# Kernel optimization log

Hardware: AMD Instinct MI355X
Metric: run time of the kernel (lower is better)

The kernel has to match this reference:

```python
import jax, jax.numpy as jnp
import numpy as np

RADIUS = 0.2
MAX_SAMPLES = 32  # max_samples_per_query


def ball_query(coords, queries, radius, k):
    """coords: [B,Np,3], queries: [B,Nq,3] -> idxs: [B,Nq,k] (first-k in index order,
    empty slots filled with the first valid index, or 0 if no neighbor -- matches
    the standard PointNet++ CUDA ball_query semantics)."""
    Np = coords.shape[1]
    # squared distances [B, Nq, Np]
    diff = queries[:, :, None, :] - coords[:, None, :, :]
    d2 = jnp.sum(diff * diff, axis=-1)
    mask = d2 < radius * radius
    # keys: point index if in-ball else sentinel Np; smallest k keys = first k valid indices
    keys = jnp.where(mask, jnp.arange(Np, dtype=jnp.int32), Np)
    neg_top, _ = jax.lax.top_k(-keys, k)           # largest of -keys == smallest keys
    sorted_keys = -neg_top                          # [B, Nq, k], ascending
    valid = sorted_keys < Np
    first = jnp.where(valid[..., 0:1], sorted_keys[..., 0:1], 0)
    return jnp.where(valid, sorted_keys, first)


def setup_inputs() -> dict:
    key = jax.random.key(0)
    k1, k2, k3, k4 = jax.random.split(key, 4)
    B, Np, Nq, C, Ct = 4, 8192, 2048, 64, 64
    return {
        "points_coords": jax.random.uniform(k1, (B, Np, 3), dtype=jnp.float32),
        "points_features": jax.random.normal(k2, (B, C, Np), dtype=jnp.float32),
        "points_t_embed": jax.random.normal(k3, (B, Ct, Np), dtype=jnp.float32),
        "queries": jax.random.uniform(k4, (B, Nq, 3), dtype=jnp.float32),
    }


def reference(points_coords, points_features, points_t_embed, queries):
    B, Np, _ = points_coords.shape
    Nq = queries.shape[1]
    K = MAX_SAMPLES
    idxs = ball_query(points_coords, queries, RADIUS, K)          # [B,Nq,K] int32
    flat = idxs.reshape(B, Nq * K)
    # grouped coords: gather along point dim then center on queries -> [B,Nq,K,3]
    grouped_coords = jnp.take_along_axis(points_coords, flat[:, :, None], axis=1)
    grouped_coords = grouped_coords.reshape(B, Nq, K, 3) - queries[:, :, None, :]
    # grouped features: gather channel-first along point dim -> [B,C,Nq,K]
    C = points_features.shape[1]
    grouped_features = jnp.take_along_axis(points_features, flat[:, None, :], axis=2)
    grouped_features = grouped_features.reshape(B, C, Nq, K)
    # use_coords=True: prepend centered coords as channels
    grouped_features = jnp.concatenate(
        [grouped_coords.transpose(0, 3, 1, 2), grouped_features], axis=1)  # [B,3+C,Nq,K]
    # t_embed gather -> [B,Ct,Nq,K]
    Ct = points_t_embed.shape[1]
    t_embed = jnp.take_along_axis(points_t_embed, flat[:, None, :], axis=2)
    t_embed = t_embed.reshape(B, Ct, Nq, K)
    return grouped_features, t_embed
```

## Files before the change

### kernel.cpp

```cpp
#include <hip/hip_runtime.h>

constexpr int kB  = 4;
constexpr int kNp = 8192;
constexpr int kNq = 2048;
constexpr int kK  = 32;
constexpr float kR2 = (float)(0.2 * 0.2);

__global__ __launch_bounds__(256) void coords_soa_kernel(
    const float* __restrict__ coords, float* __restrict__ cb3)
{
    const int t = blockIdx.x * 256 + threadIdx.x;
    const int b = t >> 13;
    const int p = t & (kNp - 1);
    const float x = coords[(size_t)t * 3 + 0];
    const float y = coords[(size_t)t * 3 + 1];
    const float z = coords[(size_t)t * 3 + 2];
    float* o = cb3 + (size_t)b * 3 * kNp;
    o[0 * kNp + p] = x;
    o[1 * kNp + p] = y;
    o[2 * kNp + p] = z;
}

__global__ __launch_bounds__(256) void ball_query_kernel(
    const float* __restrict__ cb3,
    const float* __restrict__ queries,
    int* __restrict__ idxs,
    float* __restrict__ out)
{
    const int wave = (int)((blockIdx.x * blockDim.x + threadIdx.x) >> 6);
    const int lane = threadIdx.x & 63;
    const int w    = threadIdx.x >> 6;
    const int b    = wave >> 11;
    const int q    = wave & (kNq - 1);

    const float qx = queries[(b * kNq + q) * 3 + 0];
    const float qy = queries[(b * kNq + q) * 3 + 1];
    const float qz = queries[(b * kNq + q) * 3 + 2];

    const float* __restrict__ cbx = cb3 + (size_t)b * 3 * kNp;
    const float* __restrict__ cby = cbx + kNp;
    const float* __restrict__ cbz = cby + kNp;

    __shared__ int s_idx[4][kK];

    const unsigned long long lt = (1ull << lane) - 1ull;
    int cnt = 0;
    for (int base = 0; base < kNp; base += 256) {
#pragma unroll
        for (int j = 0; j < 4; ++j) {
            const int p = base + j * 64 + lane;
            const float cx = cbx[p];
            const float cy = cby[p];
            const float cz = cbz[p];
            const float dx = __fsub_rn(qx, cx);
            const float dy = __fsub_rn(qy, cy);
            const float dz = __fsub_rn(qz, cz);
            const float d2 = __fadd_rn(
                __fadd_rn(__fmul_rn(dx, dx), __fmul_rn(dy, dy)),
                __fmul_rn(dz, dz));
            const bool in_ball = d2 < kR2;
            const unsigned long long m = __ballot(in_ball);
            if (in_ball) {
                const int slot = cnt + __popcll(m & lt);
                if (slot < kK) s_idx[w][slot] = p;
            }
            cnt += __popcll(m);
        }
        if (cnt >= kK) break;
    }

    if (lane < kK) {
        int v;
        if (cnt == 0)        v = 0;
        else if (lane < cnt) v = s_idx[w][lane];
        else                 v = s_idx[w][0];
        idxs[(size_t)wave * kK + lane] = v;

        const int k = lane;
        float* gf = out + ((size_t)(b * 67) * kNq + q) * kK + k;
        gf[(size_t)0 * kNq * kK] = __fsub_rn(cbx[v], qx);
        gf[(size_t)1 * kNq * kK] = __fsub_rn(cby[v], qy);
        gf[(size_t)2 * kNq * kK] = __fsub_rn(cbz[v], qz);
    }
}

__global__ __launch_bounds__(256) void gather_kernel(
    const float* __restrict__ feat,
    const float* __restrict__ temb,
    const int*   __restrict__ idxs,
    float* __restrict__ out)
{
    const int blk = blockIdx.x;
    const int b   = blk >> 7;
    const int j   = blk & 127;

    const float* src;
    float* dst;
    if (j < 64) {
        src = feat + ((size_t)b * 64 + j) * kNp;
        dst = out + (size_t)(b * 67 + 3 + j) * (kNq * kK);
    } else {
        src = temb + ((size_t)b * 64 + (j - 64)) * kNp;
        dst = out + (size_t)kB * 67 * kNq * kK
                  + (size_t)(b * 64 + (j - 64)) * (kNq * kK);
    }

    __shared__ float row[kNp];
    {
        const float4* s4 = (const float4*)src;
        float4* r4 = (float4*)row;
#pragma unroll
        for (int i = 0; i < kNp / 4 / 256; ++i)
            r4[i * 256 + threadIdx.x] = s4[i * 256 + threadIdx.x];
    }
    __syncthreads();

    const int4* id4 = (const int4*)(idxs + (size_t)b * kNq * kK);
    float4* d4 = (float4*)dst;
    constexpr int total4 = kNq * kK / 4;
#pragma unroll 4
    for (int e = threadIdx.x; e < total4; e += 256) {
        const int4 id = id4[e];
        float4 v;
        v.x = row[id.x];
        v.y = row[id.y];
        v.z = row[id.z];
        v.w = row[id.w];
        d4[e] = v;
    }
}

extern "C" void kernel_launch(void* const* d_in, const int* in_sizes, int n_in,
                              void* d_out, int out_size, void* d_ws, size_t ws_size,
                              hipStream_t stream) {
    const float* coords  = (const float*)d_in[0];
    const float* feats   = (const float*)d_in[1];
    const float* temb    = (const float*)d_in[2];
    const float* queries = (const float*)d_in[3];
    float* out = (float*)d_out;

    int*   idxs = (int*)d_ws;
    float* cb3  = (float*)((char*)d_ws + (size_t)kB * kNq * kK * 4);

    coords_soa_kernel<<<kB * kNp / 256, 256, 0, stream>>>(coords, cb3);
    ball_query_kernel<<<kB * kNq / 4, 256, 0, stream>>>(cb3, queries, idxs, out);
    gather_kernel<<<kB * 128, 256, 0, stream>>>(feats, temb, idxs, out);
}
```

Before: 185.2 us.

## Drop SoA coords pass, split gather rows across two blocks, use nontemporal stores

```diff
diff --git a/kernel.cpp b/kernel.cpp
--- a/kernel.cpp
+++ b/kernel.cpp
@@ -6,23 +6,11 @@
 constexpr int kK  = 32;
 constexpr float kR2 = (float)(0.2 * 0.2);
 
-__global__ __launch_bounds__(256) void coords_soa_kernel(
-    const float* __restrict__ coords, float* __restrict__ cb3)
-{
-    const int t = blockIdx.x * 256 + threadIdx.x;
-    const int b = t >> 13;
-    const int p = t & (kNp - 1);
-    const float x = coords[(size_t)t * 3 + 0];
-    const float y = coords[(size_t)t * 3 + 1];
-    const float z = coords[(size_t)t * 3 + 2];
-    float* o = cb3 + (size_t)b * 3 * kNp;
-    o[0 * kNp + p] = x;
-    o[1 * kNp + p] = y;
-    o[2 * kNp + p] = z;
-}
+typedef float v4f __attribute__((ext_vector_type(4)));
+typedef int   v4i __attribute__((ext_vector_type(4)));
 
 __global__ __launch_bounds__(256) void ball_query_kernel(
-    const float* __restrict__ cb3,
+    const float* __restrict__ coords,
     const float* __restrict__ queries,
     int* __restrict__ idxs,
     float* __restrict__ out)
@@ -37,9 +25,7 @@
     const float qy = queries[(b * kNq + q) * 3 + 1];
     const float qz = queries[(b * kNq + q) * 3 + 2];
 
-    const float* __restrict__ cbx = cb3 + (size_t)b * 3 * kNp;
-    const float* __restrict__ cby = cbx + kNp;
-    const float* __restrict__ cbz = cby + kNp;
+    const float* __restrict__ cb = coords + (size_t)b * kNp * 3;
 
     __shared__ int s_idx[4][kK];
 
@@ -49,9 +35,9 @@
 #pragma unroll
         for (int j = 0; j < 4; ++j) {
             const int p = base + j * 64 + lane;
-            const float cx = cbx[p];
-            const float cy = cby[p];
-            const float cz = cbz[p];
+            const float cx = cb[p * 3 + 0];
+            const float cy = cb[p * 3 + 1];
+            const float cz = cb[p * 3 + 2];
             const float dx = __fsub_rn(qx, cx);
             const float dy = __fsub_rn(qy, cy);
             const float dz = __fsub_rn(qz, cz);
@@ -78,9 +64,9 @@
 
         const int k = lane;
         float* gf = out + ((size_t)(b * 67) * kNq + q) * kK + k;
-        gf[(size_t)0 * kNq * kK] = __fsub_rn(cbx[v], qx);
-        gf[(size_t)1 * kNq * kK] = __fsub_rn(cby[v], qy);
-        gf[(size_t)2 * kNq * kK] = __fsub_rn(cbz[v], qz);
+        gf[(size_t)0 * kNq * kK] = __fsub_rn(cb[v * 3 + 0], qx);
+        gf[(size_t)1 * kNq * kK] = __fsub_rn(cb[v * 3 + 1], qy);
+        gf[(size_t)2 * kNq * kK] = __fsub_rn(cb[v * 3 + 2], qz);
     }
 }
 
@@ -91,8 +77,9 @@
     float* __restrict__ out)
 {
     const int blk = blockIdx.x;
-    const int b   = blk >> 7;
-    const int j   = blk & 127;
+    const int h   = blk & 1;
+    const int j   = (blk >> 1) & 127;
+    const int b   = blk >> 8;
 
     const float* src;
     float* dst;
@@ -107,26 +94,27 @@
 
     __shared__ float row[kNp];
     {
-        const float4* s4 = (const float4*)src;
-        float4* r4 = (float4*)row;
+        const v4f* s4 = (const v4f*)src;
+        v4f* r4 = (v4f*)row;
 #pragma unroll
         for (int i = 0; i < kNp / 4 / 256; ++i)
             r4[i * 256 + threadIdx.x] = s4[i * 256 + threadIdx.x];
     }
     __syncthreads();
 
-    const int4* id4 = (const int4*)(idxs + (size_t)b * kNq * kK);
-    float4* d4 = (float4*)dst;
-    constexpr int total4 = kNq * kK / 4;
+    const v4i* id4 = (const v4i*)(idxs + (size_t)b * kNq * kK);
+    v4f* d4 = (v4f*)dst;
+    constexpr int half4 = kNq * kK / 4 / 2;
+    const int e0 = h * half4;
 #pragma unroll 4
-    for (int e = threadIdx.x; e < total4; e += 256) {
-        const int4 id = id4[e];
-        float4 v;
+    for (int e = threadIdx.x; e < half4; e += 256) {
+        const v4i id = id4[e0 + e];
+        v4f v;
         v.x = row[id.x];
         v.y = row[id.y];
         v.z = row[id.z];
         v.w = row[id.w];
-        d4[e] = v;
+        __builtin_nontemporal_store(v, &d4[e0 + e]);
     }
 }
 
@@ -139,10 +127,8 @@
     const float* queries = (const float*)d_in[3];
     float* out = (float*)d_out;
 
-    int*   idxs = (int*)d_ws;
-    float* cb3  = (float*)((char*)d_ws + (size_t)kB * kNq * kK * 4);
+    int* idxs = (int*)d_ws;
 
-    coords_soa_kernel<<<kB * kNp / 256, 256, 0, stream>>>(coords, cb3);
-    ball_query_kernel<<<kB * kNq / 4, 256, 0, stream>>>(cb3, queries, idxs, out);
-    gather_kernel<<<kB * 128, 256, 0, stream>>>(feats, temb, idxs, out);
+    ball_query_kernel<<<kB * kNq / 4, 256, 0, stream>>>(coords, queries, idxs, out);
+    gather_kernel<<<kB * 128 * 2, 256, 0, stream>>>(feats, temb, idxs, out);
 }
```

Measured after the change: 201.6 us. 1.09x slower.
